# Optimization experiments

Hardware: AMD Instinct MI355X
Metric: run time of the kernel (lower is better)

Reference implementation:

```python
import jax, jax.numpy as jnp
import numpy as np

jax.config.update("jax_enable_x64", True)  # int64 pairing keys, as in the torch code

N_ATOMS = 50000
DEG_HALF = 16           # undirected edges per atom on average -> E = 2*N*16 = 1.6M
D_FEAT = 128
H_DIM = 64
KEY_SCALE = 1e10        # matches (10000000000 * x).long() in the original


def setup_inputs() -> dict:
    rng = np.random.default_rng(0)
    half = N_ATOMS * DEG_HALF
    c = rng.integers(0, N_ATOMS, half)
    n = rng.integers(0, N_ATOMS, half)
    n = np.where(n == c, (n + 1) % N_ATOMS, n)
    c[0], n[0] = N_ATOMS - 1, 0  # guarantee atom N-1 appears as a center
    # scale vectors so int64 keys have a wide range (avoids pairing-key collisions)
    v = (rng.standard_normal((half, 3)) * 50.0).astype(np.float32)
    center = np.concatenate([c, n])
    neigh = np.concatenate([n, c])
    vec = np.concatenate([v, -v], axis=0)  # reverse edge has negated vector, same length
    order = np.argsort(center, kind="stable")  # edge_center sorted -> edge_center[-1] is max
    center, neigh, vec = center[order], neigh[order], vec[order]
    lengths = np.linalg.norm(vec.astype(np.float64), axis=1).astype(np.float32)

    E = 2 * half
    k = jax.random.key(0)
    kf, k1, k2, k3, k4 = jax.random.split(k, 5)
    feats = jax.random.normal(kf, (E, D_FEAT), jnp.float32)
    w1 = jax.random.normal(k1, (D_FEAT, H_DIM), jnp.float32) / np.sqrt(D_FEAT)
    b1 = jax.random.normal(k2, (H_DIM,), jnp.float32) * 0.01
    w2 = jax.random.normal(k3, (H_DIM, 1), jnp.float32) / np.sqrt(H_DIM)
    b2 = jax.random.normal(k4, (1,), jnp.float32) * 0.01
    return {
        "features": feats,
        "edge_vectors": jnp.asarray(vec, jnp.float32),
        "edge_lengths": jnp.asarray(lengths, jnp.float32),
        "edge_index": jnp.asarray(np.stack([center, neigh]), jnp.int64),
        "w1": w1, "b1": b1, "w2": w2, "b2": b2,
    }


def _forward(features, edge_vectors, edge_lengths, edge_index, w1, b1, w2, b2):
    center = edge_index[0]
    neigh = edge_index[1]
    # per-edge MLP: Linear -> ShiftedSoftplus -> Linear(->1)
    ssp = lambda x: jax.nn.softplus(x) - jnp.log(2.0).astype(x.dtype)
    h = ssp(features @ w1 + b1)
    mag = h @ w2 + b2  # [E, 1]
    # scatter-mean debias per center atom
    ones = jnp.ones_like(mag[:, 0])
    cnt = jax.ops.segment_sum(ones, center, num_segments=N_ATOMS)
    bias = jax.ops.segment_sum(mag[:, 0], center, num_segments=N_ATOMS) / jnp.maximum(cnt, 1.0)
    mag = mag - bias[center][:, None]
    unit_vec = edge_vectors / edge_lengths[:, None]
    # ghost-atom branch: inputs are built so edge_neighbor <= max(edge_center); no ghosts.
    # sorted-pair averaging (no_grad key, E even -> argsort().view(-1, 2))
    ul = jax.lax.stop_gradient(edge_lengths)
    uv = jax.lax.stop_gradient(unit_vec)
    key_i = (center.astype(jnp.int64) + neigh.astype(jnp.int64)
             + (KEY_SCALE * ul).astype(jnp.int64)
             + (KEY_SCALE * jnp.abs(uv).sum(axis=1)).astype(jnp.int64))
    idx = jnp.argsort(key_i)
    pairs = idx.reshape(-1, 2)
    avg = 0.5 * (mag[pairs[:, 0]] + mag[pairs[:, 1]])
    mag = mag.at[pairs[:, 0]].set(avg).at[pairs[:, 1]].set(avg)
    edge_force = mag * unit_vec  # [E, 3]
    forces = jax.ops.segment_sum(edge_force, center, num_segments=N_ATOMS)
    return forces


def reference(features, edge_vectors, edge_lengths, edge_index, w1, b1, w2, b2):
    return _forward(features, edge_vectors, edge_lengths, edge_index, w1, b1, w2, b2)
```

## Files before the change

kernel.cpp:

```cpp
#include <hip/hip_runtime.h>

typedef __bf16 bf16x8 __attribute__((ext_vector_type(8)));
typedef float f32x4 __attribute__((ext_vector_type(4)));

#define DFEAT 128
#define HDIM 64
#define IDX_BITS 21
#define IDX_MASK ((1u << IDX_BITS) - 1)
#define EMPTY_SLOT 0xFFFFFFFFFFFFFFFFull

__device__ __forceinline__ float ssp_fast(float x) {
    float m = fmaxf(x, 0.0f);
    float t = __expf(-fabsf(x));
    return m + __logf(1.0f + t) - 0.69314718055994531f;
}

__global__ void detect_idx_kernel(const unsigned int* __restrict__ p, int n_check,
                                  unsigned int* __restrict__ flag_any) {
    unsigned int acc = 0;
    for (int i = threadIdx.x; i < n_check; i += blockDim.x)
        acc |= p[2 * i + 1];
    if (acc) atomicOr(flag_any, 1u);
}

__device__ __forceinline__ int load_idx(const void* p, int is64, long long i) {
    if (is64) return (int)((const long long*)p)[i];
    return ((const int*)p)[i];
}

#define CVT8H(P, Q, H) do { \
    H[0] = (__bf16)P.x; H[1] = (__bf16)P.y; H[2] = (__bf16)P.z; H[3] = (__bf16)P.w; \
    H[4] = (__bf16)Q.x; H[5] = (__bf16)Q.y; H[6] = (__bf16)Q.z; H[7] = (__bf16)Q.w; \
} while (0)

#define MF(A, B, C) __builtin_amdgcn_mfma_f32_16x16x32_bf16(A, B, C, 0, 0, 0)

#define KSTEP(P, Q, KT) do { \
    bf16x8 h, bh; \
    CVT8H(P, Q, h); \
    bh = hiTab[((KT)*4 + 0) * 64 + lane]; acc0 = MF(h, bh, acc0); \
    bh = hiTab[((KT)*4 + 1) * 64 + lane]; acc1 = MF(h, bh, acc1); \
    bh = hiTab[((KT)*4 + 2) * 64 + lane]; acc2 = MF(h, bh, acc2); \
    bh = hiTab[((KT)*4 + 3) * 64 + lane]; acc3 = MF(h, bh, acc3); \
} while (0)

#define REDJ(J, OUT) do { \
    float z0 = acc0[J] + b1v0, z1 = acc1[J] + b1v1; \
    float z2 = acc2[J] + b1v2, z3 = acc3[J] + b1v3; \
    float t = ssp_fast(z0) * w2v0 + ssp_fast(z1) * w2v1 \
            + ssp_fast(z2) * w2v2 + ssp_fast(z3) * w2v3; \
    t += __shfl_xor(t, 1); t += __shfl_xor(t, 2); \
    t += __shfl_xor(t, 4); t += __shfl_xor(t, 8); \
    OUT = t; \
} while (0)

__global__ __launch_bounds__(256, 4) void mlp_mag_kernel(
    const float* __restrict__ feats,
    const float* __restrict__ w1,
    const float* __restrict__ b1,
    const float* __restrict__ w2,
    const float* __restrict__ b2,
    float* __restrict__ mag_raw,
    int E)
{
    __shared__ __align__(16) unsigned char smem[32768];
    float* w1s = (float*)smem;
    bf16x8* hiTab = (bf16x8*)smem;

    const int lane = threadIdx.x & 63;
    const int r = lane & 15;
    const int g = lane >> 4;
    const int wave = blockIdx.x * (blockDim.x >> 6) + (threadIdx.x >> 6);
    const int nwaves = gridDim.x * (blockDim.x >> 6);

    for (int idx = threadIdx.x; idx < DFEAT * HDIM / 4; idx += blockDim.x)
        ((float4*)w1s)[idx] = ((const float4*)w1)[idx];
    __syncthreads();
    {
        const int tkt = threadIdx.x >> 6;
        const int tl = threadIdx.x & 63;
        const int tg = tl >> 4, tr = tl & 15;
        float vals[4][8];
#pragma unroll
        for (int nt = 0; nt < 4; ++nt)
#pragma unroll
            for (int i = 0; i < 8; ++i)
                vals[nt][i] = w1s[(tkt * 32 + tg * 8 + i) * HDIM + nt * 16 + tr];
        __syncthreads();
#pragma unroll
        for (int nt = 0; nt < 4; ++nt) {
            bf16x8 h;
#pragma unroll
            for (int i = 0; i < 8; ++i) h[i] = (__bf16)vals[nt][i];
            hiTab[(tkt * 4 + nt) * 64 + tl] = h;
        }
        __syncthreads();
    }

    const float b1v0 = b1[0 * 16 + r], b1v1 = b1[1 * 16 + r];
    const float b1v2 = b1[2 * 16 + r], b1v3 = b1[3 * 16 + r];
    const float w2v0 = w2[0 * 16 + r], w2v1 = w2[1 * 16 + r];
    const float w2v2 = w2[2 * 16 + r], w2v3 = w2[3 * 16 + r];
    const float b2v = b2[0];

    const int ntiles = (E + 15) >> 4;
    for (int tile = wave; tile < ntiles; tile += nwaves) {
        const int e0 = tile << 4;
        int er = e0 + r;
        if (er >= E) er = E - 1;

        const float4* fp = (const float4*)(feats + (size_t)er * DFEAT) + g * 2;
        float4 p0 = fp[0],  p1 = fp[1];
        float4 p2 = fp[8],  p3 = fp[9];
        float4 p4 = fp[16], p5 = fp[17];
        float4 p6 = fp[24], p7 = fp[25];

        f32x4 acc0 = {0.f,0.f,0.f,0.f}, acc1 = {0.f,0.f,0.f,0.f};
        f32x4 acc2 = {0.f,0.f,0.f,0.f}, acc3 = {0.f,0.f,0.f,0.f};
        KSTEP(p0, p1, 0);
        KSTEP(p2, p3, 1);
        KSTEP(p4, p5, 2);
        KSTEP(p6, p7, 3);

        float s0, s1, s2, s3;
        REDJ(0, s0); REDJ(1, s1); REDJ(2, s2); REDJ(3, s3);

        if (r < 4) {
            int e = e0 + g * 4 + r;
            if (e < E) {
                float sel = (r == 0) ? s0 : (r == 1) ? s1 : (r == 2) ? s2 : s3;
                mag_raw[e] = sel + b2v;
            }
        }
    }
}

__global__ __launch_bounds__(256) void bias_kernel(
    const void* __restrict__ eidx,
    const float* __restrict__ mag,
    float* __restrict__ csum,
    float* __restrict__ ccnt,
    const unsigned int* __restrict__ flag_any,
    int E)
{
    __shared__ int cs[256];
    __shared__ float ms[256];
    const int is64 = (flag_any[0] == 0u) ? 1 : 0;
    const int tloc = threadIdx.x;
    const int i = blockIdx.x * 256 + tloc;
    int c = -1; float m = 0.0f;
    if (i < E) { c = load_idx(eidx, is64, i); m = mag[i]; }
    cs[tloc] = c; ms[tloc] = m;
    __syncthreads();
    if (i < E) {
        bool leader = (tloc == 0) || (cs[tloc - 1] != c);
        if (leader) {
            float s = 0.0f; int n = 0; int j = tloc;
            int lim = min(256, E - blockIdx.x * 256);
            while (j < lim && cs[j] == c) { s += ms[j]; ++n; ++j; }
            atomicAdd(&csum[c], s);
            atomicAdd(&ccnt[c], (float)n);
        }
    }
}

__global__ __launch_bounds__(256) void mprime_kernel(
    const void* __restrict__ eidx,
    const float* __restrict__ mag,
    const float* __restrict__ csum,
    const float* __restrict__ ccnt,
    float* __restrict__ mprime,
    const unsigned int* __restrict__ flag_any,
    int E)
{
    int i = blockIdx.x * blockDim.x + threadIdx.x;
    if (i >= E) return;
    const int is64 = (flag_any[0] == 0u) ? 1 : 0;
    int c = load_idx(eidx, is64, i);
    mprime[i] = mag[i] - csum[c] / fmaxf(ccnt[c], 1.0f);
}

__global__ __launch_bounds__(256) void pair_kernel(
    const float* __restrict__ vec,
    const float* __restrict__ len,
    const void* __restrict__ eidx,
    const float* __restrict__ mprime,
    unsigned long long* __restrict__ tab,
    float* __restrict__ fscr,
    const unsigned int* __restrict__ flag_any,
    int E, int hash_bits)
{
    int i = blockIdx.x * blockDim.x + threadIdx.x;
    if (i >= E) return;
    const int is64 = (flag_any[0] == 0u) ? 1 : 0;

    float l = len[i];
    float ux = vec[3 * i + 0] / l;
    float uy = vec[3 * i + 1] / l;
    float uz = vec[3 * i + 2] / l;
    float s3 = (fabsf(ux) + fabsf(uy)) + fabsf(uz);

    int ci_ = load_idx(eidx, is64, i);
    int ni_ = load_idx(eidx, is64, (long long)E + i);

    long long key = (long long)ci_ + (long long)ni_
                  + (long long)(1.0e10f * l)
                  + (long long)(1.0e10f * s3);

    unsigned long long entry = ((unsigned long long)key << IDX_BITS) | (unsigned)i;
    unsigned long long h = (unsigned long long)key * 0x9E3779B97F4A7C15ull;
    unsigned slot = (unsigned)(h >> (64 - hash_bits));
    const unsigned smask = (1u << hash_bits) - 1u;

    int j;
    while (true) {
        unsigned long long old = atomicCAS(&tab[slot], EMPTY_SLOT, entry);
        if (old == EMPTY_SLOT) return;
        if ((old >> IDX_BITS) == (unsigned long long)key) {
            j = (int)(old & IDX_MASK);
            break;
        }
        slot = (slot + 1) & smask;
    }

    float avg = 0.5f * (mprime[i] + mprime[j]);
    float fx = avg * ux, fy = avg * uy, fz = avg * uz;
    fscr[3 * i + 0] = fx;   fscr[3 * i + 1] = fy;   fscr[3 * i + 2] = fz;
    fscr[3 * j + 0] = -fx;  fscr[3 * j + 1] = -fy;  fscr[3 * j + 2] = -fz;
}

__global__ __launch_bounds__(256) void force_kernel(
    const float* __restrict__ fscr,
    const void* __restrict__ eidx,
    float* __restrict__ out,
    const unsigned int* __restrict__ flag_any,
    int E)
{
    __shared__ int cs[256];
    __shared__ float fx[256], fy[256], fz[256];
    const int is64 = (flag_any[0] == 0u) ? 1 : 0;
    const int tloc = threadIdx.x;
    const int i = blockIdx.x * 256 + tloc;
    int c = -1;
    if (i < E) {
        c = load_idx(eidx, is64, i);
        fx[tloc] = fscr[3 * i + 0];
        fy[tloc] = fscr[3 * i + 1];
        fz[tloc] = fscr[3 * i + 2];
    }
    cs[tloc] = c;
    __syncthreads();
    if (i < E) {
        bool leader = (tloc == 0) || (cs[tloc - 1] != c);
        if (leader) {
            float sx = 0.f, sy = 0.f, sz = 0.f;
            int j = tloc;
            int lim = min(256, E - blockIdx.x * 256);
            while (j < lim && cs[j] == c) { sx += fx[j]; sy += fy[j]; sz += fz[j]; ++j; }
            atomicAdd(&out[c * 3 + 0], sx);
            atomicAdd(&out[c * 3 + 1], sy);
            atomicAdd(&out[c * 3 + 2], sz);
        }
    }
}

extern "C" void kernel_launch(void* const* d_in, const int* in_sizes, int n_in,
                              void* d_out, int out_size, void* d_ws, size_t ws_size,
                              hipStream_t stream) {
    const float* feats = (const float*)d_in[0];
    const float* vec   = (const float*)d_in[1];
    const float* len   = (const float*)d_in[2];
    const void*  eidx  = d_in[3];
    const float* w1 = (const float*)d_in[4];
    const float* b1 = (const float*)d_in[5];
    const float* w2 = (const float*)d_in[6];
    const float* b2 = (const float*)d_in[7];
    float* out = (float*)d_out;

    const int E = in_sizes[0] / DFEAT;
    const int N = out_size / 3;

    char* ws = (char*)d_ws;
    size_t off_mag  = 0;
    size_t off_csum = (off_mag + (size_t)E * 4 + 255) & ~(size_t)255;
    size_t off_ccnt = off_csum + (size_t)N * 4;
    size_t off_flag = (off_ccnt + (size_t)N * 4 + 255) & ~(size_t)255;
    size_t off_mpr  = off_flag + 256;
    size_t off_fscr = (off_mpr + (size_t)E * 4 + 255) & ~(size_t)255;
    size_t off_tab  = (off_fscr + (size_t)E * 12 + 255) & ~(size_t)255;

    float* mag     = (float*)(ws + off_mag);
    float* csum    = (float*)(ws + off_csum);
    float* ccnt    = (float*)(ws + off_ccnt);
    unsigned int* flag_any = (unsigned int*)(ws + off_flag);
    float* mprime  = (float*)(ws + off_mpr);
    float* fscr    = (float*)(ws + off_fscr);

    int hash_bits = 21;
    while (hash_bits > 20 && off_tab + (8ull << hash_bits) > ws_size) --hash_bits;
    unsigned long long* tab = (unsigned long long*)(ws + off_tab);

    hipMemsetAsync(csum, 0, off_flag + 256 - off_csum, stream);
    hipMemsetAsync(tab, 0xFF, (size_t)8 << hash_bits, stream);
    hipMemsetAsync(out, 0, (size_t)out_size * 4, stream);

    int n_check = E < 1024 ? E : 1024;
    detect_idx_kernel<<<1, 256, 0, stream>>>((const unsigned int*)eidx, n_check, flag_any);

    mlp_mag_kernel<<<1024, 256, 0, stream>>>(feats, w1, b1, w2, b2, mag, E);

    int eblocks = (E + 255) / 256;
    bias_kernel<<<eblocks, 256, 0, stream>>>(eidx, mag, csum, ccnt, flag_any, E);
    mprime_kernel<<<eblocks, 256, 0, stream>>>(eidx, mag, csum, ccnt, mprime, flag_any, E);
    pair_kernel<<<eblocks, 256, 0, stream>>>(vec, len, eidx, mprime,
                                             tab, fscr, flag_any, E, hash_bits);
    force_kernel<<<eblocks, 256, 0, stream>>>(fscr, eidx, out, flag_any, E);
}
```

Baseline: 327.7 us.

## Split pairing into insert/find passes keyed by center<neighbor, fuse debias

```diff
diff --git a/kernel.cpp b/kernel.cpp
--- a/kernel.cpp
+++ b/kernel.cpp
@@ -2,6 +2,7 @@
 
 typedef __bf16 bf16x8 __attribute__((ext_vector_type(8)));
 typedef float f32x4 __attribute__((ext_vector_type(4)));
+typedef unsigned long long u64x2 __attribute__((ext_vector_type(2)));
 
 #define DFEAT 128
 #define HDIM 64
@@ -29,8 +30,8 @@
 }
 
 #define CVT8H(P, Q, H) do { \
-    H[0] = (__bf16)P.x; H[1] = (__bf16)P.y; H[2] = (__bf16)P.z; H[3] = (__bf16)P.w; \
-    H[4] = (__bf16)Q.x; H[5] = (__bf16)Q.y; H[6] = (__bf16)Q.z; H[7] = (__bf16)Q.w; \
+    H[0] = (__bf16)P[0]; H[1] = (__bf16)P[1]; H[2] = (__bf16)P[2]; H[3] = (__bf16)P[3]; \
+    H[4] = (__bf16)Q[0]; H[5] = (__bf16)Q[1]; H[6] = (__bf16)Q[2]; H[7] = (__bf16)Q[3]; \
 } while (0)
 
 #define MF(A, B, C) __builtin_amdgcn_mfma_f32_16x16x32_bf16(A, B, C, 0, 0, 0)
@@ -109,11 +110,15 @@
         int er = e0 + r;
         if (er >= E) er = E - 1;
 
-        const float4* fp = (const float4*)(feats + (size_t)er * DFEAT) + g * 2;
-        float4 p0 = fp[0],  p1 = fp[1];
-        float4 p2 = fp[8],  p3 = fp[9];
-        float4 p4 = fp[16], p5 = fp[17];
-        float4 p6 = fp[24], p7 = fp[25];
+        const f32x4* fp = (const f32x4*)(feats + (size_t)er * DFEAT) + g * 2;
+        f32x4 p0 = __builtin_nontemporal_load(fp + 0);
+        f32x4 p1 = __builtin_nontemporal_load(fp + 1);
+        f32x4 p2 = __builtin_nontemporal_load(fp + 8);
+        f32x4 p3 = __builtin_nontemporal_load(fp + 9);
+        f32x4 p4 = __builtin_nontemporal_load(fp + 16);
+        f32x4 p5 = __builtin_nontemporal_load(fp + 17);
+        f32x4 p6 = __builtin_nontemporal_load(fp + 24);
+        f32x4 p7 = __builtin_nontemporal_load(fp + 25);
 
         f32x4 acc0 = {0.f,0.f,0.f,0.f}, acc1 = {0.f,0.f,0.f,0.f};
         f32x4 acc2 = {0.f,0.f,0.f,0.f}, acc3 = {0.f,0.f,0.f,0.f};
@@ -164,66 +169,100 @@
     }
 }
 
-__global__ __launch_bounds__(256) void mprime_kernel(
+__device__ __forceinline__ long long edge_key(const float* vec, float l,
+                                              int i, int ci, int ni,
+                                              float& ux, float& uy, float& uz) {
+    ux = vec[3 * i + 0] / l;
+    uy = vec[3 * i + 1] / l;
+    uz = vec[3 * i + 2] / l;
+    float s3 = (fabsf(ux) + fabsf(uy)) + fabsf(uz);
+    return (long long)ci + (long long)ni
+         + (long long)(1.0e10f * l)
+         + (long long)(1.0e10f * s3);
+}
+
+__global__ __launch_bounds__(256) void insert_kernel(
+    const float* __restrict__ vec,
+    const float* __restrict__ len,
     const void* __restrict__ eidx,
     const float* __restrict__ mag,
     const float* __restrict__ csum,
     const float* __restrict__ ccnt,
-    float* __restrict__ mprime,
+    unsigned long long* __restrict__ tab,
     const unsigned int* __restrict__ flag_any,
-    int E)
+    int E, int hash_bits)
 {
     int i = blockIdx.x * blockDim.x + threadIdx.x;
     if (i >= E) return;
     const int is64 = (flag_any[0] == 0u) ? 1 : 0;
-    int c = load_idx(eidx, is64, i);
-    mprime[i] = mag[i] - csum[c] / fmaxf(ccnt[c], 1.0f);
-}
-
-__global__ __launch_bounds__(256) void pair_kernel(
-    const float* __restrict__ vec,
-    const float* __restrict__ len,
-    const void* __restrict__ eidx,
-    const float* __restrict__ mprime,
-    unsigned long long* __restrict__ tab,
-    float* __restrict__ fscr,
-    const unsigned int* __restrict__ flag_any,
-    int E, int hash_bits)
-{
-    int i = blockIdx.x * blockDim.x + threadIdx.x;
-    if (i >= E) return;
-    const int is64 = (flag_any[0] == 0u) ? 1 : 0;
-
-    float l = len[i];
-    float ux = vec[3 * i + 0] / l;
-    float uy = vec[3 * i + 1] / l;
-    float uz = vec[3 * i + 2] / l;
-    float s3 = (fabsf(ux) + fabsf(uy)) + fabsf(uz);
 
     int ci_ = load_idx(eidx, is64, i);
     int ni_ = load_idx(eidx, is64, (long long)E + i);
-
-    long long key = (long long)ci_ + (long long)ni_
-                  + (long long)(1.0e10f * l)
-                  + (long long)(1.0e10f * s3);
+    if (ci_ >= ni_) return;
+
+    float ux, uy, uz;
+    long long key = edge_key(vec, len[i], i, ci_, ni_, ux, uy, uz);
+    float mi = mag[i] - csum[ci_] / fmaxf(ccnt[ci_], 1.0f);
 
     unsigned long long entry = ((unsigned long long)key << IDX_BITS) | (unsigned)i;
     unsigned long long h = (unsigned long long)key * 0x9E3779B97F4A7C15ull;
     unsigned slot = (unsigned)(h >> (64 - hash_bits));
     const unsigned smask = (1u << hash_bits) - 1u;
 
-    int j;
     while (true) {
-        unsigned long long old = atomicCAS(&tab[slot], EMPTY_SLOT, entry);
-        if (old == EMPTY_SLOT) return;
-        if ((old >> IDX_BITS) == (unsigned long long)key) {
-            j = (int)(old & IDX_MASK);
+        unsigned long long old = atomicCAS(&tab[2 * (size_t)slot], EMPTY_SLOT, entry);
+        if (old == EMPTY_SLOT) {
+            *(unsigned int*)(tab + 2 * (size_t)slot + 1) = __float_as_uint(mi);
+            return;
+        }
+        slot = (slot + 1) & smask;
+    }
+}
+
+__global__ __launch_bounds__(256) void find_kernel(
+    const float* __restrict__ vec,
+    const float* __restrict__ len,
+    const void* __restrict__ eidx,
+    const float* __restrict__ mag,
+    const float* __restrict__ csum,
+    const float* __restrict__ ccnt,
+    const unsigned long long* __restrict__ tab,
+    float* __restrict__ fscr,
+    const unsigned int* __restrict__ flag_any,
+    int E, int hash_bits)
+{
+    int i = blockIdx.x * blockDim.x + threadIdx.x;
+    if (i >= E) return;
+    const int is64 = (flag_any[0] == 0u) ? 1 : 0;
+
+    int ci_ = load_idx(eidx, is64, i);
+    int ni_ = load_idx(eidx, is64, (long long)E + i);
+    if (ci_ <= ni_) return;
+
+    float ux, uy, uz;
+    long long key = edge_key(vec, len[i], i, ci_, ni_, ux, uy, uz);
+    float mi = mag[i] - csum[ci_] / fmaxf(ccnt[ci_], 1.0f);
+
+    unsigned long long h = (unsigned long long)key * 0x9E3779B97F4A7C15ull;
+    unsigned slot = (unsigned)(h >> (64 - hash_bits));
+    const unsigned smask = (1u << hash_bits) - 1u;
+    const u64x2* t2 = (const u64x2*)tab;
+
+    int j = -1;
+    float mj = 0.0f;
+    int guard = (int)smask + 1;
+    while (guard-- > 0) {
+        u64x2 e = t2[slot];
+        if ((e[0] >> IDX_BITS) == (unsigned long long)key) {
+            j = (int)(e[0] & IDX_MASK);
+            mj = __uint_as_float((unsigned int)(e[1] & 0xFFFFFFFFull));
             break;
         }
         slot = (slot + 1) & smask;
     }
-
-    float avg = 0.5f * (mprime[i] + mprime[j]);
+    if (j < 0) return;
+
+    float avg = 0.5f * (mi + mj);
     float fx = avg * ux, fy = avg * uy, fz = avg * uz;
     fscr[3 * i + 0] = fx;   fscr[3 * i + 1] = fy;   fscr[3 * i + 2] = fz;
     fscr[3 * j + 0] = -fx;  fscr[3 * j + 1] = -fy;  fscr[3 * j + 2] = -fz;
@@ -285,23 +324,21 @@
     size_t off_csum = (off_mag + (size_t)E * 4 + 255) & ~(size_t)255;
     size_t off_ccnt = off_csum + (size_t)N * 4;
     size_t off_flag = (off_ccnt + (size_t)N * 4 + 255) & ~(size_t)255;
-    size_t off_mpr  = off_flag + 256;
-    size_t off_fscr = (off_mpr + (size_t)E * 4 + 255) & ~(size_t)255;
+    size_t off_fscr = off_flag + 256;
     size_t off_tab  = (off_fscr + (size_t)E * 12 + 255) & ~(size_t)255;
 
     float* mag     = (float*)(ws + off_mag);
     float* csum    = (float*)(ws + off_csum);
     float* ccnt    = (float*)(ws + off_ccnt);
     unsigned int* flag_any = (unsigned int*)(ws + off_flag);
-    float* mprime  = (float*)(ws + off_mpr);
     float* fscr    = (float*)(ws + off_fscr);
 
     int hash_bits = 21;
-    while (hash_bits > 20 && off_tab + (8ull << hash_bits) > ws_size) --hash_bits;
+    while (hash_bits > 20 && off_tab + (16ull << hash_bits) > ws_size) --hash_bits;
     unsigned long long* tab = (unsigned long long*)(ws + off_tab);
 
     hipMemsetAsync(csum, 0, off_flag + 256 - off_csum, stream);
-    hipMemsetAsync(tab, 0xFF, (size_t)8 << hash_bits, stream);
+    hipMemsetAsync(tab, 0xFF, (size_t)16 << hash_bits, stream);
     hipMemsetAsync(out, 0, (size_t)out_size * 4, stream);
 
     int n_check = E < 1024 ? E : 1024;
@@ -311,8 +348,9 @@
 
     int eblocks = (E + 255) / 256;
     bias_kernel<<<eblocks, 256, 0, stream>>>(eidx, mag, csum, ccnt, flag_any, E);
-    mprime_kernel<<<eblocks, 256, 0, stream>>>(eidx, mag, csum, ccnt, mprime, flag_any, E);
-    pair_kernel<<<eblocks, 256, 0, stream>>>(vec, len, eidx, mprime,
+    insert_kernel<<<eblocks, 256, 0, stream>>>(vec, len, eidx, mag, csum, ccnt,
+                                               tab, flag_any, E, hash_bits);
+    find_kernel<<<eblocks, 256, 0, stream>>>(vec, len, eidx, mag, csum, ccnt,
                                              tab, fscr, flag_any, E, hash_bits);
     force_kernel<<<eblocks, 256, 0, stream>>>(fscr, eidx, out, flag_any, E);
 }
```

New measurement: 305.0 us, median of 3. 6.9% less time.
